# Kernel tuning notes

Measured on AMD Instinct MI355X. Metric: run time of the kernel, lower is better.

The kernel has to match this reference:

```python
import jax, jax.numpy as jnp
import numpy as np

PC_RANGE = np.array([-20.0, -20.0, -2.3, 20.0, 20.0, 0.9], np.float32)
GRID = np.array([0.1, 0.1, 0.1], np.float32)
K = 5                      # kernel_size
C_IN, C_OUT = 128, 128
BS, G = 8, 2000
SPATIAL = tuple(int(s) for s in ((PC_RANGE[3:] - PC_RANGE[:3]) / GRID).astype(np.int32))  # (400,400,32)


def setup_inputs() -> dict:
    key = jax.random.key(0)
    k1, k2, k3 = jax.random.split(key, 3)
    instance_feature = jax.random.normal(k1, (BS, G, C_IN), jnp.float32)
    anchor = jax.random.uniform(k2, (BS, G, 3), jnp.float32)          # normalized xyz in [0,1)
    w = jax.random.normal(k3, (K ** 3, C_IN, C_OUT), jnp.float32) * 0.02  # SubMConv3d weight, flattened offsets
    return {"instance_feature": instance_feature, "anchor": anchor, "w": w}


def _voxel_indices(anchor):
    # cartesian(): map normalized anchor xyz into the pc_range box, then voxelize.
    lo = jnp.asarray(PC_RANGE[:3])
    hi = jnp.asarray(PC_RANGE[3:])
    xyz = anchor[..., :3] * (hi - lo) + lo                 # [bs, g, 3]
    idx = ((xyz - lo) / jnp.asarray(GRID)).astype(jnp.int32)
    return idx


def reference(instance_feature, anchor, w):
    bs, g, c = instance_feature.shape
    n = bs * g
    idx = _voxel_indices(anchor).reshape(n, 3)             # [n, 3] int32 voxel coords
    bidx = jnp.repeat(jnp.arange(bs, dtype=jnp.int32), g)  # [n]
    Dx, Dy, Dz = SPATIAL

    # Rulebook substitute: dense voxel -> point-id lookup (-1 = inactive).
    grid = jnp.full((bs, Dx, Dy, Dz), -1, jnp.int32)
    grid = grid.at[bidx, idx[:, 0], idx[:, 1], idx[:, 2]].set(jnp.arange(n, dtype=jnp.int32))

    feats = instance_feature.reshape(n, c)
    r = (K - 1) // 2
    ax = jnp.arange(-r, r + 1, dtype=jnp.int32)
    offs = jnp.stack(jnp.meshgrid(ax, ax, ax, indexing="ij"), -1).reshape(-1, 3)  # [K^3, 3]
    dims = jnp.asarray([Dx, Dy, Dz], jnp.int32)

    # Submanifold conv: gather neighbor features per kernel offset, matmul, accumulate.
    def step(acc, inp):
        off, wk = inp                                       # off [3], wk [Cin, Cout]
        nb = idx + off[None, :]                             # [n, 3]
        inb = jnp.all((nb >= 0) & (nb < dims[None, :]), axis=-1)
        nbc = jnp.clip(nb, 0, dims[None, :] - 1)
        j = grid[bidx, nbc[:, 0], nbc[:, 1], nbc[:, 2]]     # [n] neighbor point id or -1
        valid = inb & (j >= 0)
        fj = jnp.where(valid[:, None], feats[jnp.clip(j, 0, n - 1)], 0.0)  # [n, Cin]
        return acc + fj @ wk, None

    out0 = jnp.zeros((n, C_OUT), feats.dtype)
    out, _ = jax.lax.scan(step, out0, (offs, w))
    return out.reshape(bs, g, C_OUT)                        # output_proj = Identity
```

## Files before the change

kernel.cpp:

```cpp
#include <hip/hip_runtime.h>
#include <stdint.h>

#define BSZ 8
#define GQ 2000
#define NPTS (BSZ * GQ)
#define CH 128
#define KOFF 125
#define TBL_BITS 16
#define TBL_SIZE (1 << TBL_BITS)
#define TBL_MASK (TBL_SIZE - 1)

struct Slot { int key; int val; };

__device__ __forceinline__ uint32_t hash_of(uint32_t k) {
    return (k * 2654435761u) >> (32 - TBL_BITS);
}

__device__ __forceinline__ int3 voxel_idx(const float* __restrict__ anchor, int i,
                                          float sx, float sy, float sz,
                                          float lx, float ly, float lz, float g) {
    float ax = anchor[i * 3 + 0];
    float ay = anchor[i * 3 + 1];
    float az = anchor[i * 3 + 2];
    float x = __fadd_rn(__fmul_rn(ax, sx), lx);
    float y = __fadd_rn(__fmul_rn(ay, sy), ly);
    float z = __fadd_rn(__fmul_rn(az, sz), lz);
    int ix = (int)__fdiv_rn(__fsub_rn(x, lx), g);
    int iy = (int)__fdiv_rn(__fsub_rn(y, ly), g);
    int iz = (int)__fdiv_rn(__fsub_rn(z, lz), g);
    return make_int3(ix, iy, iz);
}

__global__ void build_hash_kernel(const float* __restrict__ anchor,
                                  Slot* __restrict__ tab,
                                  float sx, float sy, float sz,
                                  float lx, float ly, float lz, float g,
                                  int Dx, int Dy, int Dz) {
    int i = blockIdx.x * blockDim.x + threadIdx.x;
    if (i >= NPTS) return;
    int3 v = voxel_idx(anchor, i, sx, sy, sz, lx, ly, lz, g);
    if (v.x < 0 || v.x >= Dx || v.y < 0 || v.y >= Dy || v.z < 0 || v.z >= Dz) return;
    int b = i / GQ;
    int key = ((b * Dx + v.x) * Dy + v.y) * Dz + v.z;
    uint32_t slot = hash_of((uint32_t)key);
    for (;;) {
        int prev = atomicCAS(&tab[slot].key, -1, key);
        if (prev == -1 || prev == key) {
            atomicMax(&tab[slot].val, i);
            break;
        }
        slot = (slot + 1) & TBL_MASK;
    }
}

__device__ __forceinline__ int hash_query(const Slot* __restrict__ tab, int key) {
    uint32_t slot = hash_of((uint32_t)key);
    for (;;) {
        int k = tab[slot].key;
        if (k == key) return tab[slot].val;
        if (k == -1) return -1;
        slot = (slot + 1) & TBL_MASK;
    }
}

__global__ void __launch_bounds__(CH)
sconv_kernel(const float* __restrict__ feat,
             const float* __restrict__ anchor,
             const float* __restrict__ w,
             const Slot* __restrict__ tab,
             float* __restrict__ out,
             float sx, float sy, float sz,
             float lx, float ly, float lz, float g,
             int Dx, int Dy, int Dz) {
    __shared__ int cnt;
    __shared__ int lk[KOFF];
    __shared__ int lj[KOFF];
    __shared__ float fbuf[CH];

    int i = blockIdx.x;
    int t = threadIdx.x;
    if (t == 0) cnt = 0;
    __syncthreads();

    int3 v = voxel_idx(anchor, i, sx, sy, sz, lx, ly, lz, g);
    int b = i / GQ;

    if (t < KOFF) {
        int ox = t / 25 - 2;
        int oy = (t / 5) % 5 - 2;
        int oz = t % 5 - 2;
        int nx = v.x + ox, ny = v.y + oy, nz = v.z + oz;
        if (nx >= 0 && nx < Dx && ny >= 0 && ny < Dy && nz >= 0 && nz < Dz) {
            int key = ((b * Dx + nx) * Dy + ny) * Dz + nz;
            int j = hash_query(tab, key);
            if (j >= 0) {
                int p = atomicAdd(&cnt, 1);
                lk[p] = t;
                lj[p] = j;
            }
        }
    }
    __syncthreads();

    float acc = 0.0f;
    int m = cnt;
    for (int q = 0; q < m; ++q) {
        int j = lj[q];
        int k = lk[q];
        __syncthreads();
        fbuf[t] = feat[j * CH + t];
        __syncthreads();
        const float* wk = w + k * CH * CH + t;
        #pragma unroll 16
        for (int ci = 0; ci < CH; ++ci) {
            acc = fmaf(fbuf[ci], wk[ci * CH], acc);
        }
    }
    out[i * CH + t] = acc;
}

extern "C" void kernel_launch(void* const* d_in, const int* in_sizes, int n_in,
                              void* d_out, int out_size, void* d_ws, size_t ws_size,
                              hipStream_t stream) {
    const float* feat   = (const float*)d_in[0];
    const float* anchor = (const float*)d_in[1];
    const float* w      = (const float*)d_in[2];
    float* out = (float*)d_out;
    Slot* tab = (Slot*)d_ws;

    hipMemsetAsync(d_ws, 0xFF, (size_t)TBL_SIZE * sizeof(Slot), stream);

    float lx = -20.0f, ly = -20.0f, lz = -2.3f;
    float hx =  20.0f, hy =  20.0f, hz =  0.9f;
    float sx = hx - lx, sy = hy - ly, sz = hz - lz;
    float g = 0.1f;
    int Dx = (int)(sx / g);
    int Dy = (int)(sy / g);
    int Dz = (int)(sz / g);

    build_hash_kernel<<<(NPTS + 255) / 256, 256, 0, stream>>>(
        anchor, tab, sx, sy, sz, lx, ly, lz, g, Dx, Dy, Dz);

    sconv_kernel<<<NPTS, CH, 0, stream>>>(
        feat, anchor, w, tab, out, sx, sy, sz, lx, ly, lz, g, Dx, Dy, Dz);
}
```

Baseline: 116.9 us.

## Split submanifold conv into rulebook pairgen, center-offset GEMM, and sparse scatter

Neighbor-pair generation moves into its own kernel that builds a rulebook. Center-offset pairs (almost all points) are processed by a tiled 32-row register-blocked GEMM using the center weight slice. The remaining sparse neighbor pairs go through a scatter kernel that uses atomicAdd into a zeroed output. This is meant to replace per-point blocks that reread the weight matrix with one dense batched GEMM. In exchange it adds launches, a memset of the output, atomics, and a fixed cap of 16384 on non-center pairs.

```diff
diff --git a/kernel.cpp b/kernel.cpp
--- a/kernel.cpp
+++ b/kernel.cpp
@@ -6,9 +6,17 @@
 #define NPTS (BSZ * GQ)
 #define CH 128
 #define KOFF 125
+#define KSELF 62
 #define TBL_BITS 16
 #define TBL_SIZE (1 << TBL_BITS)
 #define TBL_MASK (TBL_SIZE - 1)
+#define OTHER_CAP 16384
+#define TM 32
+
+#define WS_CNT_OFF   524288
+#define WS_P62_OFF   524544
+#define WS_POTH_OFF  652544
+#define WS_VOX_OFF   914688
 
 struct Slot { int key; int val; };
 
@@ -33,14 +41,16 @@
 
 __global__ void build_hash_kernel(const float* __restrict__ anchor,
                                   Slot* __restrict__ tab,
+                                  int4* __restrict__ voxbuf,
                                   float sx, float sy, float sz,
                                   float lx, float ly, float lz, float g,
                                   int Dx, int Dy, int Dz) {
     int i = blockIdx.x * blockDim.x + threadIdx.x;
     if (i >= NPTS) return;
     int3 v = voxel_idx(anchor, i, sx, sy, sz, lx, ly, lz, g);
+    int b = i / GQ;
+    voxbuf[i] = make_int4(v.x, v.y, v.z, b);
     if (v.x < 0 || v.x >= Dx || v.y < 0 || v.y >= Dy || v.z < 0 || v.z >= Dz) return;
-    int b = i / GQ;
     int key = ((b * Dx + v.x) * Dy + v.y) * Dz + v.z;
     uint32_t slot = hash_of((uint32_t)key);
     for (;;) {
@@ -63,60 +73,127 @@
     }
 }
 
+__global__ void pairgen_kernel(const int4* __restrict__ voxbuf,
+                               const Slot* __restrict__ tab,
+                               int* __restrict__ counters,
+                               int2* __restrict__ pairs62,
+                               int4* __restrict__ pairsOther,
+                               int Dx, int Dy, int Dz) {
+    int tid = blockIdx.x * blockDim.x + threadIdx.x;
+    if (tid >= NPTS * KOFF) return;
+    int i = tid / KOFF;
+    int k = tid - i * KOFF;
+    int4 v = voxbuf[i];
+    int ox = k / 25 - 2;
+    int oy = (k / 5) % 5 - 2;
+    int oz = k % 5 - 2;
+    int nx = v.x + ox, ny = v.y + oy, nz = v.z + oz;
+    if (nx < 0 || nx >= Dx || ny < 0 || ny >= Dy || nz < 0 || nz >= Dz) return;
+    int key = ((v.w * Dx + nx) * Dy + ny) * Dz + nz;
+    int j = hash_query(tab, key);
+    if (j < 0) return;
+    if (k == KSELF) {
+        int p = atomicAdd(&counters[0], 1);
+        pairs62[p] = make_int2(i, j);
+    } else {
+        int p = atomicAdd(&counters[1], 1);
+        if (p < OTHER_CAP) pairsOther[p] = make_int4(i, j, k, 0);
+    }
+}
+
+__global__ void __launch_bounds__(256)
+gemm62_kernel(const float* __restrict__ feat,
+              const float* __restrict__ w,
+              const int2* __restrict__ pairs62,
+              const int* __restrict__ counters,
+              float* __restrict__ out) {
+    __shared__ float As[TM * CH];
+    __shared__ int rowi[TM];
+
+    int n = counters[0];
+    int rowbase = blockIdx.x * TM;
+    int t = threadIdx.x;
+
+    for (int f = t; f < TM * 32; f += 256) {
+        int r = f >> 5;
+        int c4 = f & 31;
+        int row = rowbase + r;
+        float4 val = make_float4(0.f, 0.f, 0.f, 0.f);
+        if (row < n) {
+            int2 pr = pairs62[row];
+            if (c4 == 0) rowi[r] = pr.x;
+            val = *(const float4*)(feat + (size_t)pr.y * CH + c4 * 4);
+        } else if (c4 == 0) {
+            rowi[r] = -1;
+        }
+        *(float4*)(As + r * CH + c4 * 4) = val;
+    }
+    __syncthreads();
+
+    int tc = t & 31;
+    int tr = t >> 5;
+    int r0 = tr * 4;
+
+    float acc[4][4];
+    #pragma unroll
+    for (int a = 0; a < 4; ++a)
+        #pragma unroll
+        for (int b = 0; b < 4; ++b) acc[a][b] = 0.f;
+
+    const float* B = w + (size_t)KSELF * CH * CH + tc * 4;
+    #pragma unroll 4
+    for (int k = 0; k < CH; ++k) {
+        float4 b4 = *(const float4*)(B + (size_t)k * CH);
+        float a0 = As[(r0 + 0) * CH + k];
+        float a1 = As[(r0 + 1) * CH + k];
+        float a2 = As[(r0 + 2) * CH + k];
+        float a3 = As[(r0 + 3) * CH + k];
+        acc[0][0] = fmaf(a0, b4.x, acc[0][0]); acc[0][1] = fmaf(a0, b4.y, acc[0][1]);
+        acc[0][2] = fmaf(a0, b4.z, acc[0][2]); acc[0][3] = fmaf(a0, b4.w, acc[0][3]);
+        acc[1][0] = fmaf(a1, b4.x, acc[1][0]); acc[1][1] = fmaf(a1, b4.y, acc[1][1]);
+        acc[1][2] = fmaf(a1, b4.z, acc[1][2]); acc[1][3] = fmaf(a1, b4.w, acc[1][3]);
+        acc[2][0] = fmaf(a2, b4.x, acc[2][0]); acc[2][1] = fmaf(a2, b4.y, acc[2][1]);
+        acc[2][2] = fmaf(a2, b4.z, acc[2][2]); acc[2][3] = fmaf(a2, b4.w, acc[2][3]);
+        acc[3][0] = fmaf(a3, b4.x, acc[3][0]); acc[3][1] = fmaf(a3, b4.y, acc[3][1]);
+        acc[3][2] = fmaf(a3, b4.z, acc[3][2]); acc[3][3] = fmaf(a3, b4.w, acc[3][3]);
+    }
+
+    #pragma unroll
+    for (int rr = 0; rr < 4; ++rr) {
+        int i = rowi[r0 + rr];
+        if (i >= 0) {
+            float4 v = make_float4(acc[rr][0], acc[rr][1], acc[rr][2], acc[rr][3]);
+            *(float4*)(out + (size_t)i * CH + tc * 4) = v;
+        }
+    }
+}
+
 __global__ void __launch_bounds__(CH)
-sconv_kernel(const float* __restrict__ feat,
-             const float* __restrict__ anchor,
-             const float* __restrict__ w,
-             const Slot* __restrict__ tab,
-             float* __restrict__ out,
-             float sx, float sy, float sz,
-             float lx, float ly, float lz, float g,
-             int Dx, int Dy, int Dz) {
-    __shared__ int cnt;
-    __shared__ int lk[KOFF];
-    __shared__ int lj[KOFF];
+scatter_other_kernel(const float* __restrict__ feat,
+                     const float* __restrict__ w,
+                     const int4* __restrict__ pairsOther,
+                     const int* __restrict__ counters,
+                     float* __restrict__ out) {
     __shared__ float fbuf[CH];
-
-    int i = blockIdx.x;
+    int n = counters[1];
+    if (n > OTHER_CAP) n = OTHER_CAP;
     int t = threadIdx.x;
-    if (t == 0) cnt = 0;
-    __syncthreads();
-
-    int3 v = voxel_idx(anchor, i, sx, sy, sz, lx, ly, lz, g);
-    int b = i / GQ;
-
-    if (t < KOFF) {
-        int ox = t / 25 - 2;
-        int oy = (t / 5) % 5 - 2;
-        int oz = t % 5 - 2;
-        int nx = v.x + ox, ny = v.y + oy, nz = v.z + oz;
-        if (nx >= 0 && nx < Dx && ny >= 0 && ny < Dy && nz >= 0 && nz < Dz) {
-            int key = ((b * Dx + nx) * Dy + ny) * Dz + nz;
-            int j = hash_query(tab, key);
-            if (j >= 0) {
-                int p = atomicAdd(&cnt, 1);
-                lk[p] = t;
-                lj[p] = j;
-            }
-        }
-    }
-    __syncthreads();
-
-    float acc = 0.0f;
-    int m = cnt;
-    for (int q = 0; q < m; ++q) {
-        int j = lj[q];
-        int k = lk[q];
+    for (int p = blockIdx.x; p < n; p += gridDim.x) {
+        int4 pr = pairsOther[p];
         __syncthreads();
-        fbuf[t] = feat[j * CH + t];
+        fbuf[t] = feat[(size_t)pr.y * CH + t];
         __syncthreads();
-        const float* wk = w + k * CH * CH + t;
-        #pragma unroll 16
-        for (int ci = 0; ci < CH; ++ci) {
-            acc = fmaf(fbuf[ci], wk[ci * CH], acc);
-        }
-    }
-    out[i * CH + t] = acc;
+        const float* wk = w + (size_t)pr.z * CH * CH + t;
+        float a0 = 0.f, a1 = 0.f, a2 = 0.f, a3 = 0.f;
+        #pragma unroll 8
+        for (int c = 0; c < CH; c += 4) {
+            a0 = fmaf(fbuf[c + 0], wk[(c + 0) * CH], a0);
+            a1 = fmaf(fbuf[c + 1], wk[(c + 1) * CH], a1);
+            a2 = fmaf(fbuf[c + 2], wk[(c + 2) * CH], a2);
+            a3 = fmaf(fbuf[c + 3], wk[(c + 3) * CH], a3);
+        }
+        atomicAdd(&out[(size_t)pr.x * CH + t], (a0 + a1) + (a2 + a3));
+    }
 }
 
 extern "C" void kernel_launch(void* const* d_in, const int* in_sizes, int n_in,
@@ -126,9 +203,17 @@
     const float* anchor = (const float*)d_in[1];
     const float* w      = (const float*)d_in[2];
     float* out = (float*)d_out;
-    Slot* tab = (Slot*)d_ws;
-
-    hipMemsetAsync(d_ws, 0xFF, (size_t)TBL_SIZE * sizeof(Slot), stream);
+
+    char* ws = (char*)d_ws;
+    Slot* tab        = (Slot*)ws;
+    int*  counters   = (int*)(ws + WS_CNT_OFF);
+    int2* pairs62    = (int2*)(ws + WS_P62_OFF);
+    int4* pairsOther = (int4*)(ws + WS_POTH_OFF);
+    int4* voxbuf     = (int4*)(ws + WS_VOX_OFF);
+
+    hipMemsetAsync(tab, 0xFF, (size_t)TBL_SIZE * sizeof(Slot), stream);
+    hipMemsetAsync(counters, 0, 2 * sizeof(int), stream);
+    hipMemsetAsync(out, 0, (size_t)out_size * sizeof(float), stream);
 
     float lx = -20.0f, ly = -20.0f, lz = -2.3f;
     float hx =  20.0f, hy =  20.0f, hz =  0.9f;
@@ -139,8 +224,14 @@
     int Dz = (int)(sz / g);
 
     build_hash_kernel<<<(NPTS + 255) / 256, 256, 0, stream>>>(
-        anchor, tab, sx, sy, sz, lx, ly, lz, g, Dx, Dy, Dz);
-
-    sconv_kernel<<<NPTS, CH, 0, stream>>>(
-        feat, anchor, w, tab, out, sx, sy, sz, lx, ly, lz, g, Dx, Dy, Dz);
-}
+        anchor, tab, voxbuf, sx, sy, sz, lx, ly, lz, g, Dx, Dy, Dz);
+
+    pairgen_kernel<<<(NPTS * KOFF + 255) / 256, 256, 0, stream>>>(
+        voxbuf, tab, counters, pairs62, pairsOther, Dx, Dy, Dz);
+
+    gemm62_kernel<<<NPTS / TM, 256, 0, stream>>>(
+        feat, w, pairs62, counters, out);
+
+    scatter_other_kernel<<<1024, CH, 0, stream>>>(
+        feat, w, pairsOther, counters, out);
+}
```

After: 290.1 us. 2.48x slower.

## Tile 32 points per block with dense self-offset GEMM and sparse neighbor hits

Applied to the files above, without the earlier changes.

Replaces the one-point-per-block kernel with 32-point tiles of 256 threads, each thread holding a 4x4 register accumulator. The self offset (center voxel, almost always present) runs as a dense shared-memory tile GEMM that reuses the weight matrix across 32 rows. The few remaining neighbor hits are packed into a shared list and handled by the owning thread group reading directly from global memory. This cuts per-point block overhead and redundant weight reads, but neighbor hits now serialize the whole block over its hit count, and the packed index assumes j fits in 14 bits.

```diff
diff --git a/kernel.cpp b/kernel.cpp
--- a/kernel.cpp
+++ b/kernel.cpp
@@ -6,9 +6,13 @@
 #define NPTS (BSZ * GQ)
 #define CH 128
 #define KOFF 125
+#define KSELF 62
 #define TBL_BITS 16
 #define TBL_SIZE (1 << TBL_BITS)
 #define TBL_MASK (TBL_SIZE - 1)
+#define TM 32
+#define AS_LD 129
+#define MAXHITS (TM * 124)
 
 struct Slot { int key; int val; };
 
@@ -63,60 +67,127 @@
     }
 }
 
-__global__ void __launch_bounds__(CH)
-sconv_kernel(const float* __restrict__ feat,
-             const float* __restrict__ anchor,
-             const float* __restrict__ w,
-             const Slot* __restrict__ tab,
-             float* __restrict__ out,
-             float sx, float sy, float sz,
-             float lx, float ly, float lz, float g,
-             int Dx, int Dy, int Dz) {
-    __shared__ int cnt;
-    __shared__ int lk[KOFF];
-    __shared__ int lj[KOFF];
-    __shared__ float fbuf[CH];
-
-    int i = blockIdx.x;
+__global__ void __launch_bounds__(256)
+mega_kernel(const float* __restrict__ feat,
+            const float* __restrict__ anchor,
+            const float* __restrict__ w,
+            const Slot* __restrict__ tab,
+            float* __restrict__ out,
+            float sx, float sy, float sz,
+            float lx, float ly, float lz, float g,
+            int Dx, int Dy, int Dz) {
+    __shared__ float As[TM * AS_LD];
+    __shared__ int4  vox[TM];
+    __shared__ int   selfj[TM];
+    __shared__ int   hits[MAXHITS];
+    __shared__ int   hitcnt;
+
     int t = threadIdx.x;
-    if (t == 0) cnt = 0;
+    int rowbase = blockIdx.x * TM;
+
+    if (t == 0) hitcnt = 0;
+    if (t < TM) {
+        int i = rowbase + t;
+        int3 v = voxel_idx(anchor, i, sx, sy, sz, lx, ly, lz, g);
+        vox[t] = make_int4(v.x, v.y, v.z, i / GQ);
+        selfj[t] = -1;
+    }
     __syncthreads();
 
-    int3 v = voxel_idx(anchor, i, sx, sy, sz, lx, ly, lz, g);
-    int b = i / GQ;
-
-    if (t < KOFF) {
-        int ox = t / 25 - 2;
-        int oy = (t / 5) % 5 - 2;
-        int oz = t % 5 - 2;
+    for (int f = t; f < TM * KOFF; f += 256) {
+        int p = f / KOFF;
+        int k = f - p * KOFF;
+        int4 v = vox[p];
+        int ox = k / 25 - 2;
+        int oy = (k / 5) % 5 - 2;
+        int oz = k % 5 - 2;
         int nx = v.x + ox, ny = v.y + oy, nz = v.z + oz;
         if (nx >= 0 && nx < Dx && ny >= 0 && ny < Dy && nz >= 0 && nz < Dz) {
-            int key = ((b * Dx + nx) * Dy + ny) * Dz + nz;
+            int key = ((v.w * Dx + nx) * Dy + ny) * Dz + nz;
             int j = hash_query(tab, key);
             if (j >= 0) {
-                int p = atomicAdd(&cnt, 1);
-                lk[p] = t;
-                lj[p] = j;
+                if (k == KSELF) {
+                    selfj[p] = j;
+                } else {
+                    int pos = atomicAdd(&hitcnt, 1);
+                    hits[pos] = (p << 21) | (k << 14) | j;
+                }
             }
         }
     }
     __syncthreads();
 
-    float acc = 0.0f;
-    int m = cnt;
-    for (int q = 0; q < m; ++q) {
-        int j = lj[q];
-        int k = lk[q];
-        __syncthreads();
-        fbuf[t] = feat[j * CH + t];
-        __syncthreads();
-        const float* wk = w + k * CH * CH + t;
-        #pragma unroll 16
-        for (int ci = 0; ci < CH; ++ci) {
-            acc = fmaf(fbuf[ci], wk[ci * CH], acc);
+    for (int f = t; f < TM * 32; f += 256) {
+        int r = f >> 5;
+        int c4 = f & 31;
+        int j = selfj[r];
+        float4 val = make_float4(0.f, 0.f, 0.f, 0.f);
+        if (j >= 0) val = *(const float4*)(feat + (size_t)j * CH + c4 * 4);
+        float* dst = As + r * AS_LD + c4 * 4;
+        dst[0] = val.x; dst[1] = val.y; dst[2] = val.z; dst[3] = val.w;
+    }
+    __syncthreads();
+
+    int tc = t & 31;
+    int tr = t >> 5;
+    int r0 = tr * 4;
+
+    float acc[4][4];
+    #pragma unroll
+    for (int a = 0; a < 4; ++a)
+        #pragma unroll
+        for (int b = 0; b < 4; ++b) acc[a][b] = 0.f;
+
+    const float* B = w + (size_t)KSELF * CH * CH + tc * 4;
+    #pragma unroll 4
+    for (int k = 0; k < CH; ++k) {
+        float4 b4 = *(const float4*)(B + (size_t)k * CH);
+        float a0 = As[(r0 + 0) * AS_LD + k];
+        float a1 = As[(r0 + 1) * AS_LD + k];
+        float a2 = As[(r0 + 2) * AS_LD + k];
+        float a3 = As[(r0 + 3) * AS_LD + k];
+        acc[0][0] = fmaf(a0, b4.x, acc[0][0]); acc[0][1] = fmaf(a0, b4.y, acc[0][1]);
+        acc[0][2] = fmaf(a0, b4.z, acc[0][2]); acc[0][3] = fmaf(a0, b4.w, acc[0][3]);
+        acc[1][0] = fmaf(a1, b4.x, acc[1][0]); acc[1][1] = fmaf(a1, b4.y, acc[1][1]);
+        acc[1][2] = fmaf(a1, b4.z, acc[1][2]); acc[1][3] = fmaf(a1, b4.w, acc[1][3]);
+        acc[2][0] = fmaf(a2, b4.x, acc[2][0]); acc[2][1] = fmaf(a2, b4.y, acc[2][1]);
+        acc[2][2] = fmaf(a2, b4.z, acc[2][2]); acc[2][3] = fmaf(a2, b4.w, acc[2][3]);
+        acc[3][0] = fmaf(a3, b4.x, acc[3][0]); acc[3][1] = fmaf(a3, b4.y, acc[3][1]);
+        acc[3][2] = fmaf(a3, b4.z, acc[3][2]); acc[3][3] = fmaf(a3, b4.w, acc[3][3]);
+    }
+
+    int nh = hitcnt;
+    for (int h = 0; h < nh; ++h) {
+        int packed = hits[h];
+        int p = packed >> 21;
+        if ((p >> 2) == tr) {
+            int k = (packed >> 14) & 0x7F;
+            int j = packed & 0x3FFF;
+            const float* fj = feat + (size_t)j * CH;
+            const float* wk = w + (size_t)k * CH * CH + tc * 4;
+            #pragma unroll
+            for (int rr = 0; rr < 4; ++rr) {
+                if ((p & 3) == rr) {
+                    #pragma unroll 8
+                    for (int c = 0; c < CH; ++c) {
+                        float a = fj[c];
+                        float4 b4 = *(const float4*)(wk + (size_t)c * CH);
+                        acc[rr][0] = fmaf(a, b4.x, acc[rr][0]);
+                        acc[rr][1] = fmaf(a, b4.y, acc[rr][1]);
+                        acc[rr][2] = fmaf(a, b4.z, acc[rr][2]);
+                        acc[rr][3] = fmaf(a, b4.w, acc[rr][3]);
+                    }
+                }
+            }
         }
     }
-    out[i * CH + t] = acc;
+
+    #pragma unroll
+    for (int rr = 0; rr < 4; ++rr) {
+        int i = rowbase + r0 + rr;
+        float4 v = make_float4(acc[rr][0], acc[rr][1], acc[rr][2], acc[rr][3]);
+        *(float4*)(out + (size_t)i * CH + tc * 4) = v;
+    }
 }
 
 extern "C" void kernel_launch(void* const* d_in, const int* in_sizes, int n_in,
@@ -126,9 +197,10 @@
     const float* anchor = (const float*)d_in[1];
     const float* w      = (const float*)d_in[2];
     float* out = (float*)d_out;
+
     Slot* tab = (Slot*)d_ws;
 
-    hipMemsetAsync(d_ws, 0xFF, (size_t)TBL_SIZE * sizeof(Slot), stream);
+    hipMemsetAsync(tab, 0xFF, (size_t)TBL_SIZE * sizeof(Slot), stream);
 
     float lx = -20.0f, ly = -20.0f, lz = -2.3f;
     float hx =  20.0f, hy =  20.0f, hz =  0.9f;
@@ -141,6 +213,6 @@
     build_hash_kernel<<<(NPTS + 255) / 256, 256, 0, stream>>>(
         anchor, tab, sx, sy, sz, lx, ly, lz, g, Dx, Dy, Dz);
 
-    sconv_kernel<<<NPTS, CH, 0, stream>>>(
+    mega_kernel<<<NPTS / TM, 256, 0, stream>>>(
         feat, anchor, w, tab, out, sx, sy, sz, lx, ly, lz, g, Dx, Dy, Dz);
 }
```

After: 125.6 us. 1.07x slower.
